# Optimization experiments

Hardware: AMD Instinct MI355X
Metric: run time of the kernel (lower is better)

Reference implementation:

```python
import jax, jax.numpy as jnp
import numpy as np

NUM_TX, NUM_USER, NUM_DEV = 100000, 30000, 10000
N = NUM_TX + NUM_USER + NUM_DEV
IN_C, HID, NUM_REL, NUM_CLASSES = 128, 256, 4, 2
E = 1000000
BN_EPS = 1e-5


def rgcn_conv(x, src, dst, edge_type, rel_w, root_w, bias):
    # PyG RGCNConv (no basis decomposition, mean aggregation per relation):
    # out_i = x_i @ W_root + bias + sum_r mean_{j in N_r(i)} x_j @ W_r
    n = x.shape[0]
    xs = x[src]  # [E, C] gather once, reused across relations
    out = x @ root_w + bias
    for r in range(NUM_REL):
        m = (edge_type == r).astype(x.dtype)  # [E]
        agg = jax.ops.segment_sum(xs * m[:, None], dst, num_segments=n)  # [N, C]
        cnt = jax.ops.segment_sum(m, dst, num_segments=n)  # [N]
        out = out + (agg / jnp.maximum(cnt, 1.0)[:, None]) @ rel_w[r]
    return out


def batch_norm(x, gamma, beta):
    # training-mode BN: biased batch statistics over node dim
    mean = jnp.mean(x, axis=0)
    var = jnp.mean(jnp.square(x - mean), axis=0)
    return gamma * (x - mean) * jax.lax.rsqrt(var + BN_EPS) + beta


def setup_inputs() -> dict:
    key = jax.random.key(0)
    ks = jax.random.split(key, 16)
    s = lambda *sh: 1.0 / np.sqrt(sh[-2]) if len(sh) >= 2 else 1.0
    return {
        "x_tx": jax.random.normal(ks[0], (NUM_TX, IN_C), jnp.float32),
        "user_emb": jax.random.normal(ks[1], (NUM_USER, IN_C), jnp.float32),
        "device_emb": jax.random.normal(ks[2], (NUM_DEV, IN_C), jnp.float32),
        "rel_w1": jax.random.normal(ks[3], (NUM_REL, IN_C, HID), jnp.float32) * s(IN_C, HID),
        "root_w1": jax.random.normal(ks[4], (IN_C, HID), jnp.float32) * s(IN_C, HID),
        "bias1": jnp.zeros((HID,), jnp.float32),
        "rel_w2": jax.random.normal(ks[5], (NUM_REL, HID, HID), jnp.float32) * s(HID, HID),
        "root_w2": jax.random.normal(ks[6], (HID, HID), jnp.float32) * s(HID, HID),
        "bias2": jnp.zeros((HID,), jnp.float32),
        "bn_gamma1": jnp.ones((HID,), jnp.float32),
        "bn_beta1": jnp.zeros((HID,), jnp.float32),
        "bn_gamma2": jnp.ones((HID,), jnp.float32),
        "bn_beta2": jnp.zeros((HID,), jnp.float32),
        "cls_w": jax.random.normal(ks[7], (HID, NUM_CLASSES), jnp.float32) * s(HID, NUM_CLASSES),
        "cls_b": jnp.zeros((NUM_CLASSES,), jnp.float32),
        "edge_index": jax.random.randint(ks[8], (2, E), 0, N, jnp.int32),
        "edge_type": jax.random.randint(ks[9], (E,), 0, NUM_REL, jnp.int32),
    }


def reference(x_tx, user_emb, device_emb, rel_w1, root_w1, bias1,
              rel_w2, root_w2, bias2, bn_gamma1, bn_beta1,
              bn_gamma2, bn_beta2, cls_w, cls_b, edge_index, edge_type):
    src, dst = edge_index[0], edge_index[1]
    # concat transaction features with user/device embedding tables
    x = jnp.concatenate([x_tx, user_emb, device_emb], axis=0)  # [N, IN_C]
    # layer 1
    x = rgcn_conv(x, src, dst, edge_type, rel_w1, root_w1, bias1)
    x = jax.nn.relu(batch_norm(x, bn_gamma1, bn_beta1))
    # layer 2 (dropout is identity in eval mode)
    x = rgcn_conv(x, src, dst, edge_type, rel_w2, root_w2, bias2)
    x = jax.nn.relu(batch_norm(x, bn_gamma2, bn_beta2))
    # classify transaction nodes only
    logits = x[:NUM_TX] @ cls_w + cls_b  # [NUM_TX, 2]
    return logits
```

## Files before the change

kernel.cpp:

```cpp
#include <hip/hip_runtime.h>
#include <hip/hip_bf16.h>

#define NUM_TX   100000
#define NUM_USER 30000
#define NUM_DEV  10000
#define NN       140000
#define MP       140032
#define NSLOT    1094
#define INC      128
#define HID      256
#define NEDGE    1000000
#define BN_EPS   1e-5f
#define SCAN_NB  548
#define NPART    137
#define P1_NB    500
#define P1_CHUNK 2000
#define CH_CAP   35072

typedef __attribute__((ext_vector_type(8))) short bf16x8;
typedef __attribute__((ext_vector_type(4))) float f32x4;

__device__ __forceinline__ float b2f(unsigned short s) {
    union { unsigned int u; float f; } c; c.u = ((unsigned int)s) << 16; return c.f;
}
__device__ __forceinline__ unsigned short f2b(float f) {
    union { __hip_bfloat16 h; unsigned short s; } c; c.h = __float2bfloat16(f); return c.s;
}

__global__ void mark_ws(float* __restrict__ out, int n, float val) {
    int i = blockIdx.x * 256 + threadIdx.x;
    if (i < n) out[i] = val;
}

__global__ void count_edges(const int* __restrict__ ei, int* __restrict__ cnt) {
    int e = blockIdx.x * 256 + threadIdx.x;
    if (e >= NEDGE) return;
    atomicAdd(&cnt[ei[NEDGE + e]], 1);
}

__global__ void scan_bsum(const int* __restrict__ cnt, int* __restrict__ bsum) {
    int t = threadIdx.x;
    int i = blockIdx.x * 256 + t;
    int v = (i < NN) ? cnt[i] : 0;
    __shared__ int ls[4];
#pragma unroll
    for (int d = 32; d; d >>= 1) v += __shfl_down(v, d);
    if ((t & 63) == 0) ls[t >> 6] = v;
    __syncthreads();
    if (t == 0) bsum[blockIdx.x] = ls[0] + ls[1] + ls[2] + ls[3];
}

__global__ void scan_bscan(int* __restrict__ bsum) {
    __shared__ int ss[1024];
    int t = threadIdx.x;
    int v = (t < SCAN_NB) ? bsum[t] : 0;
    ss[t] = v;
    __syncthreads();
    for (int d = 1; d < 1024; d <<= 1) {
        int u = (t >= d) ? ss[t - d] : 0;
        __syncthreads();
        ss[t] += u;
        __syncthreads();
    }
    if (t < SCAN_NB) bsum[t] = ss[t] - v;
}

__global__ void scan_final(const int* __restrict__ cnt, const int* __restrict__ bsum,
                           int* __restrict__ off) {
    __shared__ int ss[256];
    int t = threadIdx.x;
    int i = blockIdx.x * 256 + t;
    int v = (i < NN) ? cnt[i] : 0;
    ss[t] = v;
    __syncthreads();
    for (int d = 1; d < 256; d <<= 1) {
        int u = (t >= d) ? ss[t - d] : 0;
        __syncthreads();
        ss[t] += u;
        __syncthreads();
    }
    if (i <= NN) off[i] = bsum[blockIdx.x] + ss[t] - v;
}

__global__ __launch_bounds__(256) void scatter_part1(
    const int* __restrict__ ei, const int* __restrict__ et,
    const int* __restrict__ eoff, int* __restrict__ pctr,
    unsigned long long* __restrict__ ptmp) {
    __shared__ int hist[NPART];
    __shared__ int base[NPART];
    __shared__ int runc[NPART];
    int b = blockIdx.x, t = threadIdx.x;
    int e0 = b * P1_CHUNK, e1 = e0 + P1_CHUNK;
    for (int i = t; i < NPART; i += 256) { hist[i] = 0; runc[i] = 0; }
    __syncthreads();
    for (int e = e0 + t; e < e1; e += 256)
        atomicAdd(&hist[ei[NEDGE + e] >> 10], 1);
    __syncthreads();
    if (t < NPART)
        base[t] = eoff[t << 10] + atomicAdd(&pctr[t * 16], hist[t]);
    __syncthreads();
    for (int e = e0 + t; e < e1; e += 256) {
        int dst = ei[NEDGE + e];
        int p = dst >> 10;
        int r = atomicAdd(&runc[p], 1);
        unsigned long long w = (unsigned long long)(unsigned)ei[e]
                             | ((unsigned long long)(unsigned)et[e] << 18)
                             | ((unsigned long long)(unsigned)dst << 20);
        ptmp[(size_t)base[p] + r] = w;
    }
}

__global__ __launch_bounds__(1024) void scatter_part2(
    const int* __restrict__ eoff, const unsigned long long* __restrict__ ptmp,
    int* __restrict__ sedge) {
    __shared__ int lctr[1024];
    int p = blockIdx.x, t = threadIdx.x;
    int n0 = p << 10;
    int n1 = n0 + 1024; if (n1 > NN) n1 = NN;
    lctr[t] = 0;
    __syncthreads();
    int lo = eoff[n0], hi = eoff[n1];
    for (int j = lo + t; j < hi; j += 1024) {
        unsigned long long w = ptmp[j];
        int src = (int)(w & 0x3FFFF);
        int rel = (int)((w >> 18) & 3);
        int dst = (int)(w >> 20);
        int r = atomicAdd(&lctr[dst - n0], 1);
        sedge[eoff[dst] + r] = src | (rel << 28);
    }
}

__global__ void build_x0(const float* __restrict__ xt, const float* __restrict__ ue,
                         const float* __restrict__ de, unsigned short* __restrict__ X) {
    int tid = blockIdx.x * 256 + threadIdx.x;
    int i = tid >> 5;
    int c4 = (tid & 31) << 2;
    const float* s;
    if (i < NUM_TX) s = xt + (size_t)i * INC;
    else if (i < NUM_TX + NUM_USER) s = ue + (size_t)(i - NUM_TX) * INC;
    else s = de + (size_t)(i - NUM_TX - NUM_USER) * INC;
    float4 v = *(const float4*)(s + c4);
    ushort4 o;
    o.x = f2b(v.x); o.y = f2b(v.y); o.z = f2b(v.z); o.w = f2b(v.w);
    *(ushort4*)(X + (size_t)i * INC + c4) = o;
}

__global__ void build_wt(const float* __restrict__ rootw, const float* __restrict__ relw,
                         unsigned short* __restrict__ Wt, int K, int rootK) {
    int tid = blockIdx.x * 256 + threadIdx.x;
    int n = tid / K, k = tid - n * K;
    float v = (k < rootK) ? rootw[(size_t)k * HID + n] : relw[(size_t)(k - rootK) * HID + n];
    Wt[tid] = f2b(v);
}

template<int C>
__global__ __launch_bounds__(256) void aggregate(
    const unsigned short* __restrict__ X, unsigned short* __restrict__ AGG,
    const int* __restrict__ eoff, const int* __restrict__ sedge, int m0) {
    constexpr int V = C / 64;
    int w = threadIdx.x >> 6, lane = threadIdx.x & 63;
    int i = m0 + blockIdx.x * 4 + w;
    if (i >= NN) return;
    float a0[V] = {}, a1[V] = {}, a2[V] = {}, a3[V] = {};
    int c0 = 0, c1 = 0, c2 = 0, c3 = 0;
    int b = eoff[i], e = eoff[i + 1];
    const unsigned short* Xl = X + (size_t)lane * V;
    for (int p0 = b; p0 < e; p0 += 64) {
        int nb = e - p0; if (nb > 64) nb = 64;
        int myedge = (p0 + lane < e) ? sedge[p0 + lane] : 0;
        for (int q = 0; q < nb; ++q) {
            int pe = __builtin_amdgcn_readlane(myedge, q);
            int src = pe & 0x0FFFFFFF;
            int r = pe >> 28;
            const unsigned short* row = Xl + (size_t)src * C;
            float v[V];
            if constexpr (V == 2) {
                unsigned int u = *(const unsigned int*)row;
                v[0] = b2f((unsigned short)(u & 0xFFFF));
                v[1] = b2f((unsigned short)(u >> 16));
            } else {
                ushort4 u = *(const ushort4*)row;
                v[0] = b2f(u.x); v[1] = b2f(u.y); v[2] = b2f(u.z); v[3] = b2f(u.w);
            }
            if (r == 0)      { for (int j = 0; j < V; ++j) a0[j] += v[j]; c0++; }
            else if (r == 1) { for (int j = 0; j < V; ++j) a1[j] += v[j]; c1++; }
            else if (r == 2) { for (int j = 0; j < V; ++j) a2[j] += v[j]; c2++; }
            else             { for (int j = 0; j < V; ++j) a3[j] += v[j]; c3++; }
        }
    }
    float s0 = 1.0f / (float)(c0 > 1 ? c0 : 1);
    float s1 = 1.0f / (float)(c1 > 1 ? c1 : 1);
    float s2 = 1.0f / (float)(c2 > 1 ? c2 : 1);
    float s3 = 1.0f / (float)(c3 > 1 ? c3 : 1);
    unsigned short* orow = AGG + (size_t)(i - m0) * (4 * C) + lane * V;
#pragma unroll
    for (int j = 0; j < V; ++j) {
        orow[0 * C + j] = f2b(a0[j] * s0);
        orow[1 * C + j] = f2b(a1[j] * s1);
        orow[2 * C + j] = f2b(a2[j] * s2);
        orow[3 * C + j] = f2b(a3[j] * s3);
    }
}

template<int C>
__global__ __launch_bounds__(256) void gemm_split(
    const unsigned short* __restrict__ Xg, const unsigned short* __restrict__ AGGg,
    const unsigned short* __restrict__ Wt, unsigned short* __restrict__ Cg,
    const float* __restrict__ bias, float* __restrict__ partialC, int mblocks, int m0) {
    constexpr int K = 5 * C;
    constexpr int NKT = K / 64;
    constexpr int XKT = C / 64;
    __shared__ unsigned short As[128 * 64];
    __shared__ unsigned short Bs[128 * 64];
    __shared__ float sred[2][2][4][16][2];
    int bid = blockIdx.x;
    int bm = (bid & 7) + ((bid >> 4) << 3);
    int bn = (bid >> 3) & 1;
    if (bm >= mblocks) return;
    int t = threadIdx.x;
    int lane = t & 63, w = t >> 6;
    int wr = w >> 1, wc = w & 1;
    int l15 = lane & 15, l7 = lane & 7, hi = lane >> 4;
    f32x4 acc[4][4] = {};
    const int rowA0 = bm * 128, rowB0 = bn * 128;

    auto STAGE = [&](int kt) {
#pragma unroll
        for (int it = 0; it < 4; ++it) {
            int R = it * 32 + (t >> 3);
            int sl = (t & 7) ^ (R & 7);
            const unsigned short* ga;
            if (kt < XKT)
                ga = Xg + (size_t)(m0 + rowA0 + R) * C + kt * 64 + sl * 8;
            else
                ga = AGGg + (size_t)(rowA0 + R) * (4 * C) + (kt - XKT) * 64 + sl * 8;
            __builtin_amdgcn_global_load_lds(
                (const __attribute__((address_space(1))) void*)ga,
                (__attribute__((address_space(3))) void*)(As + it * 2048 + t * 8), 16, 0, 0);
            const unsigned short* gb = Wt + (size_t)(rowB0 + R) * K + kt * 64 + sl * 8;
            __builtin_amdgcn_global_load_lds(
                (const __attribute__((address_space(1))) void*)gb,
                (__attribute__((address_space(3))) void*)(Bs + it * 2048 + t * 8), 16, 0, 0);
        }
    };

    for (int kt = 0; kt < NKT; ++kt) {
        STAGE(kt);
        asm volatile("s_waitcnt vmcnt(0)" ::: "memory");
        __builtin_amdgcn_s_barrier();
        __builtin_amdgcn_sched_barrier(0);
#pragma unroll
        for (int kk = 0; kk < 64; kk += 32) {
            bf16x8 af[4], bfr[4];
            int sl2 = (((kk >> 3) + hi) ^ l7) << 3;
#pragma unroll
            for (int f = 0; f < 4; ++f) {
                int m = wr * 64 + f * 16 + l15;
                af[f] = *(const bf16x8*)(As + m * 64 + sl2);
                int n = wc * 64 + f * 16 + l15;
                bfr[f] = *(const bf16x8*)(Bs + n * 64 + sl2);
            }
#pragma unroll
            for (int i = 0; i < 4; ++i)
#pragma unroll
                for (int j = 0; j < 4; ++j)
                    acc[i][j] = __builtin_amdgcn_mfma_f32_16x16x32_bf16(af[i], bfr[j], acc[i][j], 0, 0, 0);
        }
        __builtin_amdgcn_s_barrier();
        __builtin_amdgcn_sched_barrier(0);
    }

#pragma unroll
    for (int j = 0; j < 4; ++j) {
        int n = rowB0 + wc * 64 + j * 16 + l15;
        float bs = bias[n];
        float s = 0.f, q2 = 0.f;
#pragma unroll
        for (int i = 0; i < 4; ++i)
#pragma unroll
            for (int q = 0; q < 4; ++q) {
                int ml = rowA0 + wr * 64 + i * 16 + hi * 4 + q;
                float v = acc[i][j][q] + bs;
                Cg[(size_t)ml * HID + n] = f2b(v);
                if (m0 + ml < NN) { s += v; q2 += v * v; }
            }
        s  += __shfl_down(s, 32);  s  += __shfl_down(s, 16);
        q2 += __shfl_down(q2, 32); q2 += __shfl_down(q2, 16);
        if (lane < 16) { sred[wr][wc][j][l15][0] = s; sred[wr][wc][j][l15][1] = q2; }
    }
    __syncthreads();
    if (t < 128) {
        int wcc = t >> 6, j = (t >> 4) & 3, li = t & 15;
        float s  = sred[0][wcc][j][li][0] + sred[1][wcc][j][li][0];
        float q2 = sred[0][wcc][j][li][1] + sred[1][wcc][j][li][1];
        int slot = (m0 >> 7) + bm;
        int cg = rowB0 + t;
        partialC[(size_t)slot * 512 + cg] = s;
        partialC[(size_t)slot * 512 + 256 + cg] = q2;
    }
}

__global__ void bn_red1(const float* __restrict__ pc, float* __restrict__ t2) {
    int b = blockIdx.x;
    int ch = threadIdx.x;
    float s0 = 0.f, s1 = 0.f;
    for (int s = b; s < NSLOT; s += 64) {
        s0 += pc[(size_t)s * 512 + ch];
        s1 += pc[(size_t)s * 512 + 256 + ch];
    }
    t2[b * 512 + ch] = s0;
    t2[b * 512 + 256 + ch] = s1;
}

__global__ void bn_fin2(const float* __restrict__ t2, float* __restrict__ mi) {
    int ch = threadIdx.x;
    if (ch >= HID) return;
    float s = 0.f, q2 = 0.f;
    for (int b = 0; b < 64; ++b) {
        s += t2[b * 512 + ch];
        q2 += t2[b * 512 + 256 + ch];
    }
    float mean = s / (float)NN;
    float var = q2 / (float)NN - mean * mean;
    if (var < 0.f) var = 0.f;
    mi[ch] = mean;
    mi[HID + ch] = rsqrtf(var + BN_EPS);
}

__global__ void bn_relu(const unsigned short* __restrict__ Cin, const float* __restrict__ mi,
                        const float* __restrict__ gamma, const float* __restrict__ beta,
                        unsigned short* __restrict__ Xout) {
    int tid = blockIdx.x * 256 + threadIdx.x;
    int i = tid >> 6;
    int ch = (tid & 63) << 2;
    ushort4 v = *(const ushort4*)(Cin + (size_t)i * HID + ch);
    float vv[4] = { b2f(v.x), b2f(v.y), b2f(v.z), b2f(v.w) };
    ushort4 o;
    unsigned short* op = (unsigned short*)&o;
#pragma unroll
    for (int q = 0; q < 4; ++q) {
        int c = ch + q;
        float y = gamma[c] * (vv[q] - mi[c]) * mi[HID + c] + beta[c];
        op[q] = f2b(fmaxf(y, 0.f));
    }
    *(ushort4*)(Xout + (size_t)i * HID + ch) = o;
}

__global__ __launch_bounds__(256) void classify(
    const unsigned short* __restrict__ Cin, const float* __restrict__ mi,
    const float* __restrict__ gamma, const float* __restrict__ beta,
    const float* __restrict__ cw, const float* __restrict__ cb,
    float* __restrict__ out) {
    int w = threadIdx.x >> 6, lane = threadIdx.x & 63;
    int i = blockIdx.x * 4 + w;
    if (i >= NUM_TX) return;
    int ch = lane << 2;
    ushort4 v = *(const ushort4*)(Cin + (size_t)i * HID + ch);
    float vv[4] = { b2f(v.x), b2f(v.y), b2f(v.z), b2f(v.w) };
    float a0 = 0.f, a1 = 0.f;
#pragma unroll
    for (int q = 0; q < 4; ++q) {
        int c = ch + q;
        float y = gamma[c] * (vv[q] - mi[c]) * mi[HID + c] + beta[c];
        y = fmaxf(y, 0.f);
        a0 += y * cw[c * 2 + 0];
        a1 += y * cw[c * 2 + 1];
    }
#pragma unroll
    for (int d = 32; d; d >>= 1) { a0 += __shfl_down(a0, d); a1 += __shfl_down(a1, d); }
    if (lane == 0) {
        out[(size_t)i * 2 + 0] = a0 + cb[0];
        out[(size_t)i * 2 + 1] = a1 + cb[1];
    }
}

extern "C" void kernel_launch(void* const* d_in, const int* in_sizes, int n_in,
                              void* d_out, int out_size, void* d_ws, size_t ws_size,
                              hipStream_t stream) {
    const float* x_tx   = (const float*)d_in[0];
    const float* ue     = (const float*)d_in[1];
    const float* de     = (const float*)d_in[2];
    const float* relw1  = (const float*)d_in[3];
    const float* rootw1 = (const float*)d_in[4];
    const float* bias1  = (const float*)d_in[5];
    const float* relw2  = (const float*)d_in[6];
    const float* rootw2 = (const float*)d_in[7];
    const float* bias2  = (const float*)d_in[8];
    const float* g1     = (const float*)d_in[9];
    const float* be1    = (const float*)d_in[10];
    const float* g2     = (const float*)d_in[11];
    const float* be2    = (const float*)d_in[12];
    const float* cw     = (const float*)d_in[13];
    const float* cb     = (const float*)d_in[14];
    const int*   ei     = (const int*)d_in[15];
    const int*   et     = (const int*)d_in[16];
    float* out = (float*)d_out;
    (void)in_sizes; (void)n_in;

    char* p = (char*)d_ws;
    auto take = [&](size_t b) { char* r = p; p += (b + 255) & ~(size_t)255; return r; };
    unsigned short* X  = (unsigned short*)take((size_t)MP * HID * 2);
    unsigned short* Cb = (unsigned short*)take((size_t)MP * HID * 2);
    unsigned short* Wt1 = (unsigned short*)take((size_t)HID * 640 * 2);
    unsigned short* Wt2 = (unsigned short*)take((size_t)HID * 1280 * 2);
    int* ecnt  = (int*)take((size_t)NN * 4);
    int* eoff  = (int*)take((size_t)(NN + 1) * 4);
    int* sedge = (int*)take((size_t)NEDGE * 4);
    unsigned long long* ptmp = (unsigned long long*)take((size_t)NEDGE * 8);
    int* pctr  = (int*)take((size_t)NPART * 16 * 4);
    int* bsum  = (int*)take((size_t)SCAN_NB * 4);
    float* partialC = (float*)take((size_t)NSLOT * 512 * 4);
    float* t2red    = (float*)take((size_t)64 * 512 * 4);
    float* mi1 = (float*)take(512 * 4);
    float* mi2 = (float*)take(512 * 4);
    size_t fixed = (size_t)(p - (char*)d_ws);

    long long rem = (long long)ws_size - (long long)fixed;
    long long chv = rem / (4 * HID * 2);
    int CH = (chv >= 128) ? (int)(chv & ~127LL) : 0;
    if (CH > CH_CAP) CH = CH_CAP;
    if (CH < 128) {
        mark_ws<<<(out_size + 255) / 256, 256, 0, stream>>>(out, out_size, (float)(ws_size >> 20));
        return;
    }
    unsigned short* Achunk = (unsigned short*)take((size_t)CH * 4 * HID * 2);

    hipMemsetAsync(ecnt, 0, (size_t)NN * 4, stream);
    hipMemsetAsync(pctr, 0, (size_t)NPART * 16 * 4, stream);

    count_edges<<<(NEDGE + 255) / 256, 256, 0, stream>>>(ei, ecnt);
    scan_bsum<<<SCAN_NB, 256, 0, stream>>>(ecnt, bsum);
    scan_bscan<<<1, 1024, 0, stream>>>(bsum);
    scan_final<<<SCAN_NB, 256, 0, stream>>>(ecnt, bsum, eoff);
    scatter_part1<<<P1_NB, 256, 0, stream>>>(ei, et, eoff, pctr, ptmp);
    scatter_part2<<<NPART, 1024, 0, stream>>>(eoff, ptmp, sedge);

    build_x0<<<NN * 32 / 256, 256, 0, stream>>>(x_tx, ue, de, X);
    build_wt<<<640, 256, 0, stream>>>(rootw1, relw1, Wt1, 640, 128);
    build_wt<<<1280, 256, 0, stream>>>(rootw2, relw2, Wt2, 1280, 256);

    for (int m0 = 0; m0 < MP; m0 += CH) {
        int rows = (MP - m0 < CH) ? (MP - m0) : CH;
        int mb = rows / 128;
        int grid = ((mb * 2 + 15) / 16) * 16;
        aggregate<128><<<rows / 4, 256, 0, stream>>>(X, Achunk, eoff, sedge, m0);
        gemm_split<128><<<grid, 256, 0, stream>>>(X, Achunk, Wt1, Cb + (size_t)m0 * HID, bias1, partialC, mb, m0);
    }
    bn_red1<<<64, 256, 0, stream>>>(partialC, t2red);
    bn_fin2<<<1, 256, 0, stream>>>(t2red, mi1);
    bn_relu<<<NN * 64 / 256, 256, 0, stream>>>(Cb, mi1, g1, be1, X);

    for (int m0 = 0; m0 < MP; m0 += CH) {
        int rows = (MP - m0 < CH) ? (MP - m0) : CH;
        int mb = rows / 128;
        int grid = ((mb * 2 + 15) / 16) * 16;
        aggregate<256><<<rows / 4, 256, 0, stream>>>(X, Achunk, eoff, sedge, m0);
        gemm_split<256><<<grid, 256, 0, stream>>>(X, Achunk, Wt2, Cb + (size_t)m0 * HID, bias2, partialC, mb, m0);
    }
    bn_red1<<<64, 256, 0, stream>>>(partialC, t2red);
    bn_fin2<<<1, 256, 0, stream>>>(t2red, mi2);
    classify<<<NUM_TX / 4, 256, 0, stream>>>(Cb, mi2, g2, be2, cw, cb, out);
}
```

Before: 651.0 us.

## Build CSR offsets via partition histograms and in-block scans instead of global counting

Replaces the per-node global atomic edge count and three-kernel prefix scan with a per-partition histogram and a single-block scan over 137 partitions. Per-node offsets are then computed inside scatter_part2 with a shared-memory count and scan. This removes 1M global atomics, a large memset and several launches. The cost is an extra pass over ptmp in scatter_part2 and a 1024-wide block scan.

```diff
diff --git a/kernel.cpp b/kernel.cpp
--- a/kernel.cpp
+++ b/kernel.cpp
@@ -11,7 +11,6 @@
 #define HID      256
 #define NEDGE    1000000
 #define BN_EPS   1e-5f
-#define SCAN_NB  548
 #define NPART    137
 #define P1_NB    500
 #define P1_CHUNK 2000
@@ -32,45 +31,23 @@
     if (i < n) out[i] = val;
 }
 
-__global__ void count_edges(const int* __restrict__ ei, int* __restrict__ cnt) {
-    int e = blockIdx.x * 256 + threadIdx.x;
-    if (e >= NEDGE) return;
-    atomicAdd(&cnt[ei[NEDGE + e]], 1);
-}
-
-__global__ void scan_bsum(const int* __restrict__ cnt, int* __restrict__ bsum) {
-    int t = threadIdx.x;
-    int i = blockIdx.x * 256 + t;
-    int v = (i < NN) ? cnt[i] : 0;
-    __shared__ int ls[4];
-#pragma unroll
-    for (int d = 32; d; d >>= 1) v += __shfl_down(v, d);
-    if ((t & 63) == 0) ls[t >> 6] = v;
-    __syncthreads();
-    if (t == 0) bsum[blockIdx.x] = ls[0] + ls[1] + ls[2] + ls[3];
-}
-
-__global__ void scan_bscan(int* __restrict__ bsum) {
-    __shared__ int ss[1024];
-    int t = threadIdx.x;
-    int v = (t < SCAN_NB) ? bsum[t] : 0;
-    ss[t] = v;
-    __syncthreads();
-    for (int d = 1; d < 1024; d <<= 1) {
-        int u = (t >= d) ? ss[t - d] : 0;
-        __syncthreads();
-        ss[t] += u;
-        __syncthreads();
-    }
-    if (t < SCAN_NB) bsum[t] = ss[t] - v;
-}
-
-__global__ void scan_final(const int* __restrict__ cnt, const int* __restrict__ bsum,
-                           int* __restrict__ off) {
+__global__ __launch_bounds__(256) void part_hist(const int* __restrict__ ei,
+                                                 int* __restrict__ pcount) {
+    __shared__ int hist[NPART];
+    int b = blockIdx.x, t = threadIdx.x;
+    int e0 = b * P1_CHUNK, e1 = e0 + P1_CHUNK;
+    for (int i = t; i < NPART; i += 256) hist[i] = 0;
+    __syncthreads();
+    for (int e = e0 + t; e < e1; e += 256)
+        atomicAdd(&hist[ei[NEDGE + e] >> 10], 1);
+    __syncthreads();
+    if (t < NPART && hist[t]) atomicAdd(&pcount[t * 16], hist[t]);
+}
+
+__global__ void scan_poff(const int* __restrict__ pcount, int* __restrict__ poff) {
     __shared__ int ss[256];
     int t = threadIdx.x;
-    int i = blockIdx.x * 256 + t;
-    int v = (i < NN) ? cnt[i] : 0;
+    int v = (t < NPART) ? pcount[t * 16] : 0;
     ss[t] = v;
     __syncthreads();
     for (int d = 1; d < 256; d <<= 1) {
@@ -79,12 +56,13 @@
         ss[t] += u;
         __syncthreads();
     }
-    if (i <= NN) off[i] = bsum[blockIdx.x] + ss[t] - v;
+    if (t < NPART) poff[t] = ss[t] - v;
+    if (t == NPART - 1) poff[NPART] = ss[t];
 }
 
 __global__ __launch_bounds__(256) void scatter_part1(
     const int* __restrict__ ei, const int* __restrict__ et,
-    const int* __restrict__ eoff, int* __restrict__ pctr,
+    const int* __restrict__ poff, int* __restrict__ pctr,
     unsigned long long* __restrict__ ptmp) {
     __shared__ int hist[NPART];
     __shared__ int base[NPART];
@@ -97,7 +75,7 @@
         atomicAdd(&hist[ei[NEDGE + e] >> 10], 1);
     __syncthreads();
     if (t < NPART)
-        base[t] = eoff[t << 10] + atomicAdd(&pctr[t * 16], hist[t]);
+        base[t] = poff[t] + atomicAdd(&pctr[t * 16], hist[t]);
     __syncthreads();
     for (int e = e0 + t; e < e1; e += 256) {
         int dst = ei[NEDGE + e];
@@ -111,22 +89,38 @@
 }
 
 __global__ __launch_bounds__(1024) void scatter_part2(
-    const int* __restrict__ eoff, const unsigned long long* __restrict__ ptmp,
-    int* __restrict__ sedge) {
-    __shared__ int lctr[1024];
+    const int* __restrict__ poff, const unsigned long long* __restrict__ ptmp,
+    int* __restrict__ eoff, int* __restrict__ sedge) {
+    __shared__ int lcnt[1024];
+    __shared__ int lpre[1024];
+    __shared__ int lrun[1024];
     int p = blockIdx.x, t = threadIdx.x;
     int n0 = p << 10;
-    int n1 = n0 + 1024; if (n1 > NN) n1 = NN;
-    lctr[t] = 0;
-    __syncthreads();
-    int lo = eoff[n0], hi = eoff[n1];
+    lcnt[t] = 0; lrun[t] = 0;
+    __syncthreads();
+    int lo = poff[p], hi = poff[p + 1];
+    for (int j = lo + t; j < hi; j += 1024)
+        atomicAdd(&lcnt[(int)(ptmp[j] >> 20) - n0], 1);
+    __syncthreads();
+    int v = lcnt[t];
+    lpre[t] = v;
+    __syncthreads();
+    for (int d = 1; d < 1024; d <<= 1) {
+        int u = (t >= d) ? lpre[t - d] : 0;
+        __syncthreads();
+        lpre[t] += u;
+        __syncthreads();
+    }
+    int gi = n0 + t;
+    if (gi <= NN) eoff[gi] = lo + lpre[t] - v;
+    __syncthreads();
     for (int j = lo + t; j < hi; j += 1024) {
         unsigned long long w = ptmp[j];
         int src = (int)(w & 0x3FFFF);
         int rel = (int)((w >> 18) & 3);
-        int dst = (int)(w >> 20);
-        int r = atomicAdd(&lctr[dst - n0], 1);
-        sedge[eoff[dst] + r] = src | (rel << 28);
+        int local = (int)(w >> 20) - n0;
+        int r = atomicAdd(&lrun[local], 1);
+        sedge[lo + lpre[local] - lcnt[local] + r] = src | (rel << 28);
     }
 }
 
@@ -403,12 +397,12 @@
     unsigned short* Cb = (unsigned short*)take((size_t)MP * HID * 2);
     unsigned short* Wt1 = (unsigned short*)take((size_t)HID * 640 * 2);
     unsigned short* Wt2 = (unsigned short*)take((size_t)HID * 1280 * 2);
-    int* ecnt  = (int*)take((size_t)NN * 4);
     int* eoff  = (int*)take((size_t)(NN + 1) * 4);
     int* sedge = (int*)take((size_t)NEDGE * 4);
     unsigned long long* ptmp = (unsigned long long*)take((size_t)NEDGE * 8);
-    int* pctr  = (int*)take((size_t)NPART * 16 * 4);
-    int* bsum  = (int*)take((size_t)SCAN_NB * 4);
+    int* pcount = (int*)take((size_t)NPART * 16 * 4);
+    int* pctr   = (int*)take((size_t)NPART * 16 * 4);
+    int* poff   = (int*)take((size_t)(NPART + 1) * 4);
     float* partialC = (float*)take((size_t)NSLOT * 512 * 4);
     float* t2red    = (float*)take((size_t)64 * 512 * 4);
     float* mi1 = (float*)take(512 * 4);
@@ -425,15 +419,13 @@
     }
     unsigned short* Achunk = (unsigned short*)take((size_t)CH * 4 * HID * 2);
 
-    hipMemsetAsync(ecnt, 0, (size_t)NN * 4, stream);
+    hipMemsetAsync(pcount, 0, (size_t)NPART * 16 * 4, stream);
     hipMemsetAsync(pctr, 0, (size_t)NPART * 16 * 4, stream);
 
-    count_edges<<<(NEDGE + 255) / 256, 256, 0, stream>>>(ei, ecnt);
-    scan_bsum<<<SCAN_NB, 256, 0, stream>>>(ecnt, bsum);
-    scan_bscan<<<1, 1024, 0, stream>>>(bsum);
-    scan_final<<<SCAN_NB, 256, 0, stream>>>(ecnt, bsum, eoff);
-    scatter_part1<<<P1_NB, 256, 0, stream>>>(ei, et, eoff, pctr, ptmp);
-    scatter_part2<<<NPART, 1024, 0, stream>>>(eoff, ptmp, sedge);
+    part_hist<<<P1_NB, 256, 0, stream>>>(ei, pcount);
+    scan_poff<<<1, 256, 0, stream>>>(pcount, poff);
+    scatter_part1<<<P1_NB, 256, 0, stream>>>(ei, et, poff, pctr, ptmp);
+    scatter_part2<<<NPART, 1024, 0, stream>>>(poff, ptmp, eoff, sedge);
 
     build_x0<<<NN * 32 / 256, 256, 0, stream>>>(x_tx, ue, de, X);
     build_wt<<<640, 256, 0, stream>>>(rootw1, relw1, Wt1, 640, 128);
```

Measured after the change: 621.8 us (median of 2 runs). 1.05x faster.
